# Kernel optimization log

Hardware: AMD Instinct MI355X
Metric: run time of the kernel (lower is better)

Reference implementation:

```python
import jax, jax.numpy as jnp
import numpy as np

N = 100_000      # num nodes
E = 100_000      # num hyperedges
NNZ = 1_600_000  # incidence entries (avg degree 16)
DIN = 128
DOUT = 128


def setup_inputs() -> dict:
    key = jax.random.key(0)
    k1, k2, k3, k4 = jax.random.split(key, 4)
    x = jax.random.normal(k1, (N, DIN), dtype=jnp.float32)
    weight = jax.random.normal(k2, (DIN, DOUT), dtype=jnp.float32) / np.sqrt(DIN).astype(np.float32)
    bias = jax.random.normal(k3, (DOUT,), dtype=jnp.float32) * 0.02
    hyperedge_index = jax.random.randint(k4, (2, NNZ), 0, N, dtype=jnp.int64)
    return {"x": x, "weight": weight, "bias": bias, "hyperedge_index": hyperedge_index}


def reference(x, weight, bias, hyperedge_index):
    # PyG HypergraphConv (use_attention=False, heads=1):
    #   out = D^{-1} H W B^{-1} H^T (x @ Theta) + bias, W = I (unit hyperedge weights)
    node_idx = hyperedge_index[0]  # [NNZ]
    edge_idx = hyperedge_index[1]  # [NNZ]

    h = x @ weight  # [N, DOUT]

    ones = jnp.ones((NNZ,), dtype=h.dtype)
    # node degree D_i = sum of hyperedge weights (=1) over incident hyperedges
    D = jax.ops.segment_sum(ones, node_idx, num_segments=N)   # [N]
    # hyperedge degree B_e = number of incident nodes
    B = jax.ops.segment_sum(ones, edge_idx, num_segments=E)   # [E]
    Dinv = jnp.where(D > 0, 1.0 / D, 0.0)
    Binv = jnp.where(B > 0, 1.0 / B, 0.0)

    # nodes -> hyperedges: m_e = B_e^{-1} * sum_{i in e} h_i
    e_feat = jax.ops.segment_sum(h[node_idx], edge_idx, num_segments=E) * Binv[:, None]  # [E, DOUT]
    # hyperedges -> nodes: out_i = D_i^{-1} * sum_{e ni i} m_e
    out = jax.ops.segment_sum(e_feat[edge_idx], node_idx, num_segments=N) * Dinv[:, None]  # [N, DOUT]
    return out + bias
```

## Files before the change

### kernel.cpp

```cpp
#include <hip/hip_runtime.h>

#define Nn 100000
#define Ne 100000
#define NNZC 1600000
#define NBLK 256
#define CHUNK 6250
#define BSH 7
#define BUCKW 128
#define NBK 782
#define SCANSZ (NBK * NBLK)

typedef __attribute__((ext_vector_type(8))) short short8;
typedef __attribute__((ext_vector_type(4))) float floatx4;

__device__ inline float bf2f(unsigned short u) {
    union { unsigned int i; float f; } c; c.i = ((unsigned int)u) << 16; return c.f;
}
__device__ inline unsigned short f2bf(float f) {
    union { float f; unsigned int i; } c; c.f = f;
    unsigned int i = c.i;
    return (unsigned short)((i + 0x7fffu + ((i >> 16) & 1u)) >> 16);
}
__device__ inline unsigned int f2bf2(float lo, float hi) {
    union { float f; unsigned int i; } a, b;
    a.f = lo; b.f = hi;
    const unsigned int x = (a.i + 0x7fffu + ((a.i >> 16) & 1u)) >> 16;
    const unsigned int y = (b.i + 0x7fffu + ((b.i >> 16) & 1u)) & 0xffff0000u;
    return x | y;
}

__global__ void hist_kernel(const int* __restrict__ nidx, const int* __restrict__ eidx,
                            int* __restrict__ histN, int* __restrict__ histE) {
    __shared__ int hN[NBK], hE[NBK];
    for (int j = threadIdx.x; j < NBK; j += 256) { hN[j] = 0; hE[j] = 0; }
    __syncthreads();
    const int base = blockIdx.x * CHUNK;
    for (int i = base + threadIdx.x; i < base + CHUNK; i += 256) {
        atomicAdd(&hN[nidx[i] >> BSH], 1);
        atomicAdd(&hE[eidx[i] >> BSH], 1);
    }
    __syncthreads();
    for (int j = threadIdx.x; j < NBK; j += 256) {
        histN[j * NBLK + blockIdx.x] = hN[j];
        histE[j * NBLK + blockIdx.x] = hE[j];
    }
}

__global__ void scan1_kernel(int* __restrict__ histN, int* __restrict__ histE,
                             int* __restrict__ bsumN, int* __restrict__ bsumE) {
    const int arr = blockIdx.x / NBK;
    const int b = blockIdx.x % NBK;
    int* a = arr ? histE : histN;
    int* bs = arr ? bsumE : bsumN;
    const int t = threadIdx.x;
    int v = a[b * 256 + t];
    __shared__ int tmp[2][256];
    int pin = 0;
    tmp[0][t] = v;
    for (int off = 1; off < 256; off <<= 1) {
        __syncthreads();
        int val = tmp[pin][t];
        if (t >= off) val += tmp[pin][t - off];
        tmp[1 - pin][t] = val;
        pin ^= 1;
    }
    __syncthreads();
    int incl = tmp[pin][t];
    a[b * 256 + t] = incl - v;
    if (t == 255) bs[b] = incl;
}

__global__ void scan2_kernel(int* __restrict__ bsumN, int* __restrict__ bsumE) {
    int* bs = blockIdx.x ? bsumE : bsumN;
    const int t = threadIdx.x;
    int v = (t < NBK) ? bs[t] : 0;
    __shared__ int tmp[2][1024];
    int pin = 0;
    tmp[0][t] = v;
    for (int off = 1; off < 1024; off <<= 1) {
        __syncthreads();
        int val = tmp[pin][t];
        if (t >= off) val += tmp[pin][t - off];
        tmp[1 - pin][t] = val;
        pin ^= 1;
    }
    __syncthreads();
    if (t < NBK) bs[t] = tmp[pin][t] - v;
}

__global__ void scan3_kernel(int* __restrict__ histN, int* __restrict__ histE,
                             const int* __restrict__ bsumN, const int* __restrict__ bsumE) {
    const int arr = blockIdx.x / NBK;
    const int b = blockIdx.x % NBK;
    int* a = arr ? histE : histN;
    const int* bs = arr ? bsumE : bsumN;
    a[b * 256 + threadIdx.x] += bs[b];
}

__global__ void scatter_kernel(const int* __restrict__ nidx, const int* __restrict__ eidx,
                               const int* __restrict__ histN, const int* __restrict__ histE,
                               int2* __restrict__ pairsN, int2* __restrict__ pairsE) {
    __shared__ int cN[NBK], cE[NBK];
    const int blk = blockIdx.x;
    for (int j = threadIdx.x; j < NBK; j += 256) {
        cN[j] = histN[j * NBLK + blk];
        cE[j] = histE[j * NBLK + blk];
    }
    __syncthreads();
    const int base = blk * CHUNK;
    for (int i = base + threadIdx.x; i < base + CHUNK; i += 256) {
        const int n = nidx[i], e = eidx[i];
        const int pn = atomicAdd(&cN[n >> BSH], 1);
        const int pe = atomicAdd(&cE[e >> BSH], 1);
        pairsN[pn] = make_int2(n, e);
        pairsE[pe] = make_int2(e, n);
    }
}

__global__ void fine_kernel(const int2* __restrict__ pairsN, const int2* __restrict__ pairsE,
                            const int* __restrict__ histN, const int* __restrict__ histE,
                            int* __restrict__ offsN, int* __restrict__ offsE,
                            int* __restrict__ permN, int* __restrict__ permE) {
    const int arr = blockIdx.x / NBK;
    const int b = blockIdx.x % NBK;
    const int2* pairs = arr ? pairsE : pairsN;
    const int* hist = arr ? histE : histN;
    int* offs = arr ? offsE : offsN;
    int* perm = arr ? permE : permN;
    const int t = threadIdx.x;
    const int S = hist[b * NBLK];
    const int E = (b + 1 < NBK) ? hist[(b + 1) * NBLK] : NNZC;
    __shared__ int cnt[BUCKW];
    __shared__ int tmp[2][BUCKW];
    cnt[t] = 0;
    __syncthreads();
    for (int i = S + t; i < E; i += BUCKW)
        atomicAdd(&cnt[pairs[i].x & (BUCKW - 1)], 1);
    __syncthreads();
    int v = cnt[t];
    int pin = 0;
    tmp[0][t] = v;
    for (int off = 1; off < BUCKW; off <<= 1) {
        __syncthreads();
        int val = tmp[pin][t];
        if (t >= off) val += tmp[pin][t - off];
        tmp[1 - pin][t] = val;
        pin ^= 1;
    }
    __syncthreads();
    const int excl = tmp[pin][t] - v;
    const int id = b * BUCKW + t;
    if (id < 100000) offs[id] = S + excl;
    if (b == NBK - 1 && t == 0) offs[100000] = NNZC;
    __syncthreads();
    cnt[t] = excl;
    __syncthreads();
    for (int i = S + t; i < E; i += BUCKW) {
        const int2 p = pairs[i];
        const int pos = S + atomicAdd(&cnt[p.x & (BUCKW - 1)], 1);
        perm[pos] = p.y;
    }
}

__global__ __launch_bounds__(256) void gemm_mfma_kernel(const float* __restrict__ x,
                                                        const float* __restrict__ w,
                                                        unsigned short* __restrict__ h) {
    __shared__ unsigned short wlds[128 * 136];
    __shared__ unsigned short tile[4][16 * 136];
    const int tid = threadIdx.x;
    const int wave = tid >> 6, lane = tid & 63;
    const int q = lane >> 4, r16 = lane & 15;

    for (int i = tid; i < 4096; i += 256) {
        const int k = i >> 5;
        const int n0 = (i & 31) << 2;
        const float4 wv = *(const float4*)(w + k * 128 + n0);
        wlds[(n0 + 0) * 136 + k] = f2bf(wv.x);
        wlds[(n0 + 1) * 136 + k] = f2bf(wv.y);
        wlds[(n0 + 2) * 136 + k] = f2bf(wv.z);
        wlds[(n0 + 3) * 136 + k] = f2bf(wv.w);
    }
    __syncthreads();

    const int row0 = blockIdx.x * 64 + wave * 16;
    if (row0 >= Nn) return;

    floatx4 acc[8];
#pragma unroll
    for (int jb = 0; jb < 8; ++jb) acc[jb] = (floatx4){0.f, 0.f, 0.f, 0.f};

    const float* ap = x + (size_t)(row0 + r16) * 128 + q * 8;
#pragma unroll
    for (int kk = 0; kk < 4; ++kk) {
        const float4 a0 = *(const float4*)(ap + kk * 32);
        const float4 a1 = *(const float4*)(ap + kk * 32 + 4);
        union { unsigned int u[4]; short8 s; } af;
        af.u[0] = f2bf2(a0.x, a0.y);
        af.u[1] = f2bf2(a0.z, a0.w);
        af.u[2] = f2bf2(a1.x, a1.y);
        af.u[3] = f2bf2(a1.z, a1.w);
        const unsigned short* wp = wlds + kk * 32 + q * 8;
#pragma unroll
        for (int jb = 0; jb < 8; ++jb) {
            const short8 bfr = *(const short8*)(wp + (jb * 16 + r16) * 136);
            acc[jb] = __builtin_amdgcn_mfma_f32_16x16x32_bf16(af.s, bfr, acc[jb], 0, 0, 0);
        }
    }

    unsigned short* tw = tile[wave];
#pragma unroll
    for (int jb = 0; jb < 8; ++jb)
#pragma unroll
        for (int r = 0; r < 4; ++r)
            tw[(q * 4 + r) * 136 + jb * 16 + r16] = f2bf(acc[jb][r]);

    const int rr = lane >> 2, seg = lane & 3;
    const unsigned short* src = tw + rr * 136 + seg * 32;
    unsigned short* dst = h + (size_t)(row0 + rr) * 128 + seg * 32;
    *(short8*)(dst + 0)  = *(const short8*)(src + 0);
    *(short8*)(dst + 8)  = *(const short8*)(src + 8);
    *(short8*)(dst + 16) = *(const short8*)(src + 16);
    *(short8*)(dst + 24) = *(const short8*)(src + 24);
}

__device__ inline void gather_rows(const ushort2* __restrict__ src, const int* __restrict__ perm,
                                   int start, int end, int lane, float& ax, float& ay) {
    for (int s0 = start; s0 < end; s0 += 64) {
        const int m = min(end - s0, 64);
        const int myv = perm[s0 + (lane < m ? lane : 0)];
        for (int t = 0; t < m; t += 4) {
            const int i1 = (t + 1 < m) ? t + 1 : t;
            const int i2 = (t + 2 < m) ? t + 2 : t;
            const int i3 = (t + 3 < m) ? t + 3 : t;
            const int n0 = __shfl(myv, t, 64);
            const int n1 = __shfl(myv, i1, 64);
            const int n2 = __shfl(myv, i2, 64);
            const int n3 = __shfl(myv, i3, 64);
            const ushort2 v0 = src[(size_t)n0 * 64 + lane];
            const ushort2 v1 = src[(size_t)n1 * 64 + lane];
            const ushort2 v2 = src[(size_t)n2 * 64 + lane];
            const ushort2 v3 = src[(size_t)n3 * 64 + lane];
            const float f1 = (t + 1 < m) ? 1.f : 0.f;
            const float f2 = (t + 2 < m) ? 1.f : 0.f;
            const float f3 = (t + 3 < m) ? 1.f : 0.f;
            ax += bf2f(v0.x) + f1 * bf2f(v1.x) + f2 * bf2f(v2.x) + f3 * bf2f(v3.x);
            ay += bf2f(v0.y) + f1 * bf2f(v1.y) + f2 * bf2f(v2.y) + f3 * bf2f(v3.y);
        }
    }
}

__global__ void gather_n2e_kernel(const int* __restrict__ perm, const int* __restrict__ offs,
                                  const unsigned short* __restrict__ h,
                                  unsigned short* __restrict__ ef) {
    const int wave = threadIdx.x >> 6;
    const int lane = threadIdx.x & 63;
    const int e = blockIdx.x * 4 + wave;
    const int start = offs[e], end = offs[e + 1];
    float ax = 0.f, ay = 0.f;
    gather_rows((const ushort2*)h, perm, start, end, lane, ax, ay);
    const int deg = end - start;
    const float binv = deg ? 1.f / (float)deg : 0.f;
    ushort2 o;
    o.x = f2bf(ax * binv);
    o.y = f2bf(ay * binv);
    ((ushort2*)ef)[(size_t)e * 64 + lane] = o;
}

__global__ void gather_e2n_kernel(const int* __restrict__ perm, const int* __restrict__ offs,
                                  const unsigned short* __restrict__ ef,
                                  const float* __restrict__ bias,
                                  float* __restrict__ out) {
    const int wave = threadIdx.x >> 6;
    const int lane = threadIdx.x & 63;
    const int n = blockIdx.x * 4 + wave;
    const int start = offs[n], end = offs[n + 1];
    float ax = 0.f, ay = 0.f;
    gather_rows((const ushort2*)ef, perm, start, end, lane, ax, ay);
    const int deg = end - start;
    const float dinv = deg ? 1.f / (float)deg : 0.f;
    const float2 b = ((const float2*)bias)[lane];
    float2 o;
    o.x = ax * dinv + b.x;
    o.y = ay * dinv + b.y;
    ((float2*)out)[(size_t)n * 64 + lane] = o;
}

extern "C" void kernel_launch(void* const* d_in, const int* in_sizes, int n_in,
                              void* d_out, int out_size, void* d_ws, size_t ws_size,
                              hipStream_t stream) {
    const float* x = (const float*)d_in[0];
    const float* w = (const float*)d_in[1];
    const float* bias = (const float*)d_in[2];
    const int* hei = (const int*)d_in[3];
    const int* nidx = hei;
    const int* eidx = hei + NNZC;
    float* out = (float*)d_out;

    char* p = (char*)d_ws;
    unsigned short* h = (unsigned short*)p;  p += (size_t)Nn * 128 * 2;
    unsigned short* ef = (unsigned short*)p; p += (size_t)Ne * 128 * 2;
    int* histN = (int*)p;                    p += (size_t)SCANSZ * 4;
    int* histE = (int*)p;                    p += (size_t)SCANSZ * 4;
    int* bsumN = (int*)p;                    p += 3328;
    int* bsumE = (int*)p;                    p += 3328;
    int* offsN = (int*)p;                    p += 400128;
    int* offsE = (int*)p;                    p += 400128;
    int* permN = (int*)p;                    p += (size_t)NNZC * 4;
    int* permE = (int*)p;                    p += (size_t)NNZC * 4;
    int2* pairsN = (int2*)p;                 p += (size_t)NNZC * 8;
    int2* pairsE = (int2*)p;                 p += (size_t)NNZC * 8;

    gemm_mfma_kernel<<<(Nn + 63) / 64, 256, 0, stream>>>(x, w, h);

    hist_kernel<<<NBLK, 256, 0, stream>>>(nidx, eidx, histN, histE);
    scan1_kernel<<<2 * NBK, 256, 0, stream>>>(histN, histE, bsumN, bsumE);
    scan2_kernel<<<2, 1024, 0, stream>>>(bsumN, bsumE);
    scan3_kernel<<<2 * NBK, 256, 0, stream>>>(histN, histE, bsumN, bsumE);
    scatter_kernel<<<NBLK, 256, 0, stream>>>(nidx, eidx, histN, histE, pairsN, pairsE);
    fine_kernel<<<2 * NBK, BUCKW, 0, stream>>>(pairsN, pairsE, histN, histE,
                                               offsN, offsE, permN, permE);

    gather_n2e_kernel<<<Ne / 4, 256, 0, stream>>>(permE, offsE, h, ef);
    gather_e2n_kernel<<<Nn / 4, 256, 0, stream>>>(permN, offsN, ef, bias, out);
}
```

Before: 338.0 us.

## Widen sort buckets, pack sort pairs to 32 bits, drop scan2, streamline gather

Bucket width for the counting sort doubles to 256, which halves the number of coarse buckets. Each scatter pair is packed into one 32-bit word (partner index shifted left 8, low byte of the key) instead of an int2, halving pair traffic. The separate block-sum scan kernel is removed; scan3 instead reduces the preceding block sums itself. The gather loop drops the masked-multiply tail handling in favour of a clean unrolled body plus a remainder loop, and uses 32-bit byte-offset addressing. The packing assumes indices below 2^24, and the fine sort block now has 256 threads.

New measurement: 320.9 us. -5.1%, faster.

```diff
diff --git a/kernel.cpp b/kernel.cpp
--- a/kernel.cpp
+++ b/kernel.cpp
@@ -5,17 +5,13 @@
 #define NNZC 1600000
 #define NBLK 256
 #define CHUNK 6250
-#define BSH 7
-#define BUCKW 128
-#define NBK 782
-#define SCANSZ (NBK * NBLK)
+#define BSH 8
+#define BUCKW 256
+#define NBK 391
 
 typedef __attribute__((ext_vector_type(8))) short short8;
 typedef __attribute__((ext_vector_type(4))) float floatx4;
 
-__device__ inline float bf2f(unsigned short u) {
-    union { unsigned int i; float f; } c; c.i = ((unsigned int)u) << 16; return c.f;
-}
 __device__ inline unsigned short f2bf(float f) {
     union { float f; unsigned int i; } c; c.f = f;
     unsigned int i = c.i;
@@ -70,36 +66,28 @@
     if (t == 255) bs[b] = incl;
 }
 
-__global__ void scan2_kernel(int* __restrict__ bsumN, int* __restrict__ bsumE) {
-    int* bs = blockIdx.x ? bsumE : bsumN;
-    const int t = threadIdx.x;
-    int v = (t < NBK) ? bs[t] : 0;
-    __shared__ int tmp[2][1024];
-    int pin = 0;
-    tmp[0][t] = v;
-    for (int off = 1; off < 1024; off <<= 1) {
-        __syncthreads();
-        int val = tmp[pin][t];
-        if (t >= off) val += tmp[pin][t - off];
-        tmp[1 - pin][t] = val;
-        pin ^= 1;
-    }
-    __syncthreads();
-    if (t < NBK) bs[t] = tmp[pin][t] - v;
-}
-
 __global__ void scan3_kernel(int* __restrict__ histN, int* __restrict__ histE,
                              const int* __restrict__ bsumN, const int* __restrict__ bsumE) {
     const int arr = blockIdx.x / NBK;
     const int b = blockIdx.x % NBK;
     int* a = arr ? histE : histN;
     const int* bs = arr ? bsumE : bsumN;
-    a[b * 256 + threadIdx.x] += bs[b];
+    const int t = threadIdx.x;
+    int part = 0;
+    for (int i = t; i < b; i += 256) part += bs[i];
+    __shared__ int red[256];
+    red[t] = part;
+    __syncthreads();
+    for (int off = 128; off > 0; off >>= 1) {
+        if (t < off) red[t] += red[t + off];
+        __syncthreads();
+    }
+    a[b * 256 + t] += red[0];
 }
 
 __global__ void scatter_kernel(const int* __restrict__ nidx, const int* __restrict__ eidx,
                                const int* __restrict__ histN, const int* __restrict__ histE,
-                               int2* __restrict__ pairsN, int2* __restrict__ pairsE) {
+                               unsigned int* __restrict__ pairsN, unsigned int* __restrict__ pairsE) {
     __shared__ int cN[NBK], cE[NBK];
     const int blk = blockIdx.x;
     for (int j = threadIdx.x; j < NBK; j += 256) {
@@ -112,18 +100,18 @@
         const int n = nidx[i], e = eidx[i];
         const int pn = atomicAdd(&cN[n >> BSH], 1);
         const int pe = atomicAdd(&cE[e >> BSH], 1);
-        pairsN[pn] = make_int2(n, e);
-        pairsE[pe] = make_int2(e, n);
-    }
-}
-
-__global__ void fine_kernel(const int2* __restrict__ pairsN, const int2* __restrict__ pairsE,
+        pairsN[pn] = ((unsigned int)e << 8) | (unsigned int)(n & 255);
+        pairsE[pe] = ((unsigned int)n << 8) | (unsigned int)(e & 255);
+    }
+}
+
+__global__ void fine_kernel(const unsigned int* __restrict__ pairsN, const unsigned int* __restrict__ pairsE,
                             const int* __restrict__ histN, const int* __restrict__ histE,
                             int* __restrict__ offsN, int* __restrict__ offsE,
                             int* __restrict__ permN, int* __restrict__ permE) {
     const int arr = blockIdx.x / NBK;
     const int b = blockIdx.x % NBK;
-    const int2* pairs = arr ? pairsE : pairsN;
+    const unsigned int* pairs = arr ? pairsE : pairsN;
     const int* hist = arr ? histE : histN;
     int* offs = arr ? offsE : offsN;
     int* perm = arr ? permE : permN;
@@ -135,7 +123,7 @@
     cnt[t] = 0;
     __syncthreads();
     for (int i = S + t; i < E; i += BUCKW)
-        atomicAdd(&cnt[pairs[i].x & (BUCKW - 1)], 1);
+        atomicAdd(&cnt[pairs[i] & 255u], 1);
     __syncthreads();
     int v = cnt[t];
     int pin = 0;
@@ -156,9 +144,9 @@
     cnt[t] = excl;
     __syncthreads();
     for (int i = S + t; i < E; i += BUCKW) {
-        const int2 p = pairs[i];
-        const int pos = S + atomicAdd(&cnt[p.x & (BUCKW - 1)], 1);
-        perm[pos] = p.y;
+        const unsigned int p = pairs[i];
+        const int pos = S + atomicAdd(&cnt[p & 255u], 1);
+        perm[pos] = (int)(p >> 8);
     }
 }
 
@@ -223,28 +211,31 @@
     *(short8*)(dst + 24) = *(const short8*)(src + 24);
 }
 
-__device__ inline void gather_rows(const ushort2* __restrict__ src, const int* __restrict__ perm,
+__device__ inline void gather_rows(const char* __restrict__ src, const int* __restrict__ perm,
                                    int start, int end, int lane, float& ax, float& ay) {
+    const unsigned int laneoff = (unsigned int)lane << 2;
     for (int s0 = start; s0 < end; s0 += 64) {
         const int m = min(end - s0, 64);
         const int myv = perm[s0 + (lane < m ? lane : 0)];
-        for (int t = 0; t < m; t += 4) {
-            const int i1 = (t + 1 < m) ? t + 1 : t;
-            const int i2 = (t + 2 < m) ? t + 2 : t;
-            const int i3 = (t + 3 < m) ? t + 3 : t;
-            const int n0 = __shfl(myv, t, 64);
-            const int n1 = __shfl(myv, i1, 64);
-            const int n2 = __shfl(myv, i2, 64);
-            const int n3 = __shfl(myv, i3, 64);
-            const ushort2 v0 = src[(size_t)n0 * 64 + lane];
-            const ushort2 v1 = src[(size_t)n1 * 64 + lane];
-            const ushort2 v2 = src[(size_t)n2 * 64 + lane];
-            const ushort2 v3 = src[(size_t)n3 * 64 + lane];
-            const float f1 = (t + 1 < m) ? 1.f : 0.f;
-            const float f2 = (t + 2 < m) ? 1.f : 0.f;
-            const float f3 = (t + 3 < m) ? 1.f : 0.f;
-            ax += bf2f(v0.x) + f1 * bf2f(v1.x) + f2 * bf2f(v2.x) + f3 * bf2f(v3.x);
-            ay += bf2f(v0.y) + f1 * bf2f(v1.y) + f2 * bf2f(v2.y) + f3 * bf2f(v3.y);
+        int t = 0;
+        for (; t + 3 < m; t += 4) {
+            const unsigned int a0 = ((unsigned int)__shfl(myv, t, 64) << 8) | laneoff;
+            const unsigned int a1 = ((unsigned int)__shfl(myv, t + 1, 64) << 8) | laneoff;
+            const unsigned int a2 = ((unsigned int)__shfl(myv, t + 2, 64) << 8) | laneoff;
+            const unsigned int a3 = ((unsigned int)__shfl(myv, t + 3, 64) << 8) | laneoff;
+            const unsigned int u0 = *(const unsigned int*)(src + a0);
+            const unsigned int u1 = *(const unsigned int*)(src + a1);
+            const unsigned int u2 = *(const unsigned int*)(src + a2);
+            const unsigned int u3 = *(const unsigned int*)(src + a3);
+            ax += __uint_as_float(u0 << 16); ay += __uint_as_float(u0 & 0xffff0000u);
+            ax += __uint_as_float(u1 << 16); ay += __uint_as_float(u1 & 0xffff0000u);
+            ax += __uint_as_float(u2 << 16); ay += __uint_as_float(u2 & 0xffff0000u);
+            ax += __uint_as_float(u3 << 16); ay += __uint_as_float(u3 & 0xffff0000u);
+        }
+        for (; t < m; ++t) {
+            const unsigned int a0 = ((unsigned int)__shfl(myv, t, 64) << 8) | laneoff;
+            const unsigned int u0 = *(const unsigned int*)(src + a0);
+            ax += __uint_as_float(u0 << 16); ay += __uint_as_float(u0 & 0xffff0000u);
         }
     }
 }
@@ -257,13 +248,11 @@
     const int e = blockIdx.x * 4 + wave;
     const int start = offs[e], end = offs[e + 1];
     float ax = 0.f, ay = 0.f;
-    gather_rows((const ushort2*)h, perm, start, end, lane, ax, ay);
+    gather_rows((const char*)h, perm, start, end, lane, ax, ay);
     const int deg = end - start;
     const float binv = deg ? 1.f / (float)deg : 0.f;
-    ushort2 o;
-    o.x = f2bf(ax * binv);
-    o.y = f2bf(ay * binv);
-    ((ushort2*)ef)[(size_t)e * 64 + lane] = o;
+    const unsigned int o = f2bf2(ax * binv, ay * binv);
+    *(unsigned int*)((char*)ef + (((unsigned int)e << 8) | ((unsigned int)lane << 2))) = o;
 }
 
 __global__ void gather_e2n_kernel(const int* __restrict__ perm, const int* __restrict__ offs,
@@ -275,14 +264,14 @@
     const int n = blockIdx.x * 4 + wave;
     const int start = offs[n], end = offs[n + 1];
     float ax = 0.f, ay = 0.f;
-    gather_rows((const ushort2*)ef, perm, start, end, lane, ax, ay);
+    gather_rows((const char*)ef, perm, start, end, lane, ax, ay);
     const int deg = end - start;
     const float dinv = deg ? 1.f / (float)deg : 0.f;
     const float2 b = ((const float2*)bias)[lane];
     float2 o;
     o.x = ax * dinv + b.x;
     o.y = ay * dinv + b.y;
-    ((float2*)out)[(size_t)n * 64 + lane] = o;
+    *(float2*)((char*)out + (((unsigned int)n << 9) | ((unsigned int)lane << 3))) = o;
 }
 
 extern "C" void kernel_launch(void* const* d_in, const int* in_sizes, int n_in,
@@ -299,22 +288,21 @@
     char* p = (char*)d_ws;
     unsigned short* h = (unsigned short*)p;  p += (size_t)Nn * 128 * 2;
     unsigned short* ef = (unsigned short*)p; p += (size_t)Ne * 128 * 2;
-    int* histN = (int*)p;                    p += (size_t)SCANSZ * 4;
-    int* histE = (int*)p;                    p += (size_t)SCANSZ * 4;
-    int* bsumN = (int*)p;                    p += 3328;
-    int* bsumE = (int*)p;                    p += 3328;
+    int* histN = (int*)p;                    p += (size_t)NBK * NBLK * 4 + 256;
+    int* histE = (int*)p;                    p += (size_t)NBK * NBLK * 4 + 256;
+    int* bsumN = (int*)p;                    p += 1792;
+    int* bsumE = (int*)p;                    p += 1792;
     int* offsN = (int*)p;                    p += 400128;
     int* offsE = (int*)p;                    p += 400128;
     int* permN = (int*)p;                    p += (size_t)NNZC * 4;
     int* permE = (int*)p;                    p += (size_t)NNZC * 4;
-    int2* pairsN = (int2*)p;                 p += (size_t)NNZC * 8;
-    int2* pairsE = (int2*)p;                 p += (size_t)NNZC * 8;
+    unsigned int* pairsN = (unsigned int*)p; p += (size_t)NNZC * 4;
+    unsigned int* pairsE = (unsigned int*)p; p += (size_t)NNZC * 4;
 
     gemm_mfma_kernel<<<(Nn + 63) / 64, 256, 0, stream>>>(x, w, h);
 
     hist_kernel<<<NBLK, 256, 0, stream>>>(nidx, eidx, histN, histE);
     scan1_kernel<<<2 * NBK, 256, 0, stream>>>(histN, histE, bsumN, bsumE);
-    scan2_kernel<<<2, 1024, 0, stream>>>(bsumN, bsumE);
     scan3_kernel<<<2 * NBK, 256, 0, stream>>>(histN, histE, bsumN, bsumE);
     scatter_kernel<<<NBLK, 256, 0, stream>>>(nidx, eidx, histN, histE, pairsN, pairsE);
     fine_kernel<<<2 * NBK, BUCKW, 0, stream>>>(pairsN, pairsE, histN, histE,
```
